# Optimization experiments

Hardware: AMD Instinct MI355X
Metric: run time of the kernel (lower is better)

The kernel has to match this reference:

```python
import jax, jax.numpy as jnp
import numpy as np

B, S = 16, 8192
Q_DIM, K_DIM, ATTN_DIM = 512, 512, 512


def setup_inputs() -> dict:
    key = jax.random.key(0)
    k1, k2, k3, k4, k5, k6 = jax.random.split(key, 6)
    query = jax.random.normal(k1, (B, Q_DIM), dtype=jnp.float32)
    keys = jax.random.normal(k2, (B, S, K_DIM), dtype=jnp.float32)
    mask = jax.random.randint(k3, (B, S), 0, 2, dtype=jnp.int32)
    # learned params (torch Linear stores weight as [out, in]; we keep [in, out])
    Wq = jax.random.normal(k4, (Q_DIM, ATTN_DIM), dtype=jnp.float32) / np.sqrt(Q_DIM)
    Wk = jax.random.normal(k5, (K_DIM, ATTN_DIM), dtype=jnp.float32) / np.sqrt(K_DIM)
    v = jax.random.normal(k6, (ATTN_DIM,), dtype=jnp.float32) / np.sqrt(ATTN_DIM)
    return {"query": query, "keys": keys, "mask": mask, "Wq": Wq, "Wk": Wk, "v": v}


def reference(query, keys, mask, Wq, Wk, v):
    # q: [B, 1, A], k: [B, S, A]
    q = (query @ Wq)[:, None, :]
    k = jnp.einsum('bsk,ka->bsa', keys, Wk)
    # scores e: [B, S]  (v-projection reduces attn dim)
    e = jnp.einsum('bsa,a->bs', jnp.tanh(q + k), v)
    neg_min = jnp.finfo(e.dtype).min
    e = jnp.where(mask == 0, neg_min, e)
    a = jax.nn.softmax(e, axis=-1)  # [B, S]
    c = jnp.einsum('bs,bsk->bk', a, keys)  # context [B, K_DIM]
    return (c, a)
```

## Files before the change

### kernel.cpp

```cpp
#include <hip/hip_runtime.h>

#define BB 16
#define SS 8192
#define DD 512

typedef float  f32x4  __attribute__((ext_vector_type(4)));
typedef __bf16 bf16x8 __attribute__((ext_vector_type(8)));
typedef __bf16 bf16x4 __attribute__((ext_vector_type(4)));

__device__ __forceinline__ void cvt_store_bf4(unsigned short* dst, f32x4 v) {
    bf16x4 o;
    o.x = (__bf16)v.x; o.y = (__bf16)v.y; o.z = (__bf16)v.z; o.w = (__bf16)v.w;
    *(bf16x4*)dst = o;
}

__device__ __forceinline__ float tanh_fast(float x) {
    float e2 = __expf(2.0f * x);
    return 1.0f - 2.0f / (e2 + 1.0f);
}

__global__ __launch_bounds__(256) void prep_kernel(
    const float* __restrict__ query, const float* __restrict__ Wq,
    const float* __restrict__ Wk, float* __restrict__ qproj,
    unsigned short* __restrict__ WkT_f)
{
    __shared__ __bf16 lt[64][65];
    const int bid = blockIdx.x, t = threadIdx.x;
    if (bid < 64) {
        const int k0 = (bid >> 3) * 64, n0 = (bid & 7) * 64;
#pragma unroll
        for (int rep = 0; rep < 4; ++rep) {
            const int k = rep * 16 + (t >> 4), n = (t & 15) * 4;
            f32x4 vv = *(const f32x4*)&Wk[(size_t)(k0 + k) * DD + n0 + n];
            lt[k][n] = (__bf16)vv.x; lt[k][n + 1] = (__bf16)vv.y;
            lt[k][n + 2] = (__bf16)vv.z; lt[k][n + 3] = (__bf16)vv.w;
        }
        __syncthreads();
        const int g_loc = t >> 6, lane = t & 63;
        const int ml = lane & 15, quad = lane >> 4;
        const int g = (bid & 7) * 4 + g_loc;
#pragma unroll
        for (int j_loc = 0; j_loc < 2; ++j_loc) {
            const int j = (bid >> 3) * 2 + j_loc;
            bf16x8 o;
#pragma unroll
            for (int d = 0; d < 8; ++d)
                o[d] = lt[j_loc * 32 + quad * 8 + d][g_loc * 16 + ml];
            *(bf16x8*)&WkT_f[((size_t)((g * 16 + j) * 64 + lane)) * 8] = o;
        }
    } else {
        const int idx = (bid - 64) * 256 + t;
        const int b = idx >> 9;
        const int n = idx & 511;
        const float* q  = query + b * DD;
        const float* wp = Wq + n;
        float acc = 0.0f;
#pragma unroll 8
        for (int k = 0; k < DD; ++k)
            acc = fmaf(q[k], wp[(size_t)k * DD], acc);
        qproj[b * DD + n] = acc;
    }
}

__global__ __launch_bounds__(512, 4) void fused_kernel(
    const float* __restrict__ keys, const unsigned short* __restrict__ WkT_f,
    const float* __restrict__ qproj, const float* __restrict__ vvec,
    const int* __restrict__ mask, float* __restrict__ e_ws,
    float* __restrict__ cpart, float2* __restrict__ ml_ws)
{
    __shared__ unsigned short ksA[16 * 2048];
    __shared__ float sm_part[8][64];
    __shared__ float w_sh[64];
    __shared__ f32x4 red[3][128];

    const int tid  = threadIdx.x;
    const int w    = tid >> 6;
    const int lane = tid & 63;
    const int ml   = lane & 15;
    const int quad = lane >> 4;
    const int bid  = blockIdx.x;
    const int b    = bid >> 7;
    const int chunk = bid & 127;
    const int s0   = chunk << 6;

    const int m  = tid >> 3;
    const int q8 = tid & 7;
    const float* krow = keys + ((size_t)(b * SS + s0 + m)) * DD + q8 * 4;
    const int it = m >> 4;
    const int sq = q8 >> 1;
    const int j0 = (q8 & 1) * 4;
    const int base = it * 512 + ((m & 15) + 16 * sq) * 8 + j0;
    {
        f32x4 kst[8];
#pragma unroll
        for (int h = 0; h < 2; ++h) {
#pragma unroll
            for (int j = 0; j < 8; ++j)
                kst[j] = *(const f32x4*)(krow + (h * 8 + j) * 32);
#pragma unroll
            for (int j = 0; j < 8; ++j)
                cvt_store_bf4(&ksA[(h * 8 + j) * 2048 + base], kst[j]);
        }
    }
    __syncthreads();

    const unsigned short* wfb = WkT_f + (size_t)w * 32768 + lane * 8;

    f32x4 acc[4][4];
#pragma unroll
    for (int i = 0; i < 4; ++i)
#pragma unroll
        for (int jn = 0; jn < 4; ++jn) acc[i][jn] = (f32x4){0.f, 0.f, 0.f, 0.f};

#pragma unroll 4
    for (int j = 0; j < 16; ++j) {
        bf16x8 af[4];
#pragma unroll
        for (int i = 0; i < 4; ++i)
            af[i] = *(const bf16x8*)&ksA[j * 2048 + (i * 64 + lane) * 8];
#pragma unroll
        for (int jn = 0; jn < 4; ++jn) {
            bf16x8 bfr = *(const bf16x8*)(wfb + ((jn * 16 + j) << 9));
#pragma unroll
            for (int i = 0; i < 4; ++i)
                acc[i][jn] = __builtin_amdgcn_mfma_f32_16x16x32_bf16(af[i], bfr, acc[i][jn], 0, 0, 0);
        }
    }

    float qv[4], vv[4];
#pragma unroll
    for (int jn = 0; jn < 4; ++jn) {
        const int n = w * 64 + jn * 16 + ml;
        qv[jn] = qproj[b * DD + n];
        vv[jn] = vvec[n];
    }
#pragma unroll
    for (int i = 0; i < 4; ++i) {
#pragma unroll
        for (int r = 0; r < 4; ++r) {
            float s = 0.0f;
#pragma unroll
            for (int jn = 0; jn < 4; ++jn) {
                float xx = acc[i][jn][r] + qv[jn];
                s += tanh_fast(xx) * vv[jn];
            }
            s += __shfl_xor(s, 1, 64);
            s += __shfl_xor(s, 2, 64);
            s += __shfl_xor(s, 4, 64);
            s += __shfl_xor(s, 8, 64);
            if (ml == 0) sm_part[w][i * 16 + quad * 4 + r] = s;
        }
    }
    __syncthreads();

    if (tid < 64) {
        float e = sm_part[0][tid] + sm_part[1][tid] + sm_part[2][tid] + sm_part[3][tid]
                + sm_part[4][tid] + sm_part[5][tid] + sm_part[6][tid] + sm_part[7][tid];
        const int mk = mask[b * SS + s0 + tid];
        if (mk == 0) e = -3.402823466e38f;
        e_ws[(size_t)b * SS + s0 + tid] = e;
        float mx = e;
#pragma unroll
        for (int off = 32; off >= 1; off >>= 1) mx = fmaxf(mx, __shfl_xor(mx, off, 64));
        float wv = (mk == 0) ? 0.0f : __expf(e - mx);
        float l  = wv;
#pragma unroll
        for (int off = 32; off >= 1; off >>= 1) l += __shfl_xor(l, off, 64);
        w_sh[tid] = wv;
        if (tid == 0) ml_ws[b * 128 + chunk] = make_float2(mx, l);
    }
    __syncthreads();

    const int n4 = (tid & 127) << 2;
    const int sh = tid >> 7;
    const float* kctx = keys + ((size_t)(b * SS + s0 + sh * 16)) * DD + n4;
    f32x4 cacc = (f32x4){0.f, 0.f, 0.f, 0.f};
#pragma unroll 8
    for (int sI = 0; sI < 16; ++sI) {
        float wgt = w_sh[sh * 16 + sI];
        f32x4 kv  = *(const f32x4*)(kctx + (size_t)sI * DD);
        cacc += kv * wgt;
    }
    if (sh) red[sh - 1][tid & 127] = cacc;
    __syncthreads();
    if (sh == 0) {
        cacc += red[0][tid] + red[1][tid] + red[2][tid];
        *(f32x4*)(cpart + ((size_t)(b * 128 + chunk)) * 512 + n4) = cacc;
    }
}

__global__ __launch_bounds__(256) void finalize_kernel(
    const float* __restrict__ e_ws, const float* __restrict__ cpart,
    const float2* __restrict__ ml_ws, float* __restrict__ out)
{
    __shared__ float rm[4], rs[4];
    __shared__ float sc_sh[128];
    __shared__ float cred[4][512];
    const int bid = blockIdx.x, t = threadIdx.x;
    const int b = (bid < 16) ? bid : ((bid - 16) >> 3);

    float mi = -3.402823466e38f, li = 0.0f;
    if (t < 128) { float2 p = ml_ws[b * 128 + t]; mi = p.x; li = p.y; }
    float mr = mi;
#pragma unroll
    for (int off = 32; off >= 1; off >>= 1) mr = fmaxf(mr, __shfl_xor(mr, off, 64));
    if ((t & 63) == 0) rm[t >> 6] = mr;
    __syncthreads();
    const float M = fmaxf(fmaxf(rm[0], rm[1]), fmaxf(rm[2], rm[3]));
    float si = (t < 128) ? li * __expf(mi - M) : 0.0f;
#pragma unroll
    for (int off = 32; off >= 1; off >>= 1) si += __shfl_xor(si, off, 64);
    if ((t & 63) == 0) rs[t >> 6] = si;
    __syncthreads();
    const float L = rs[0] + rs[1] + rs[2] + rs[3];
    const float invL = 1.0f / L;

    if (bid < 16) {
        if (t < 128) sc_sh[t] = __expf(ml_ws[b * 128 + t].x - M);
        __syncthreads();
        const int w2 = t >> 6, l = t & 63;
        float pa[8] = {0.f, 0.f, 0.f, 0.f, 0.f, 0.f, 0.f, 0.f};
#pragma unroll 4
        for (int i = w2 * 32; i < w2 * 32 + 32; ++i) {
            const float sc = sc_sh[i];
            const float* cp = cpart + ((size_t)(b * 128 + i)) * 512 + l * 8;
#pragma unroll
            for (int c = 0; c < 8; ++c) pa[c] = fmaf(cp[c], sc, pa[c]);
        }
#pragma unroll
        for (int c = 0; c < 8; ++c) cred[w2][l * 8 + c] = pa[c];
        __syncthreads();
#pragma unroll
        for (int rep = 0; rep < 2; ++rep) {
            const int n = t + rep * 256;
            out[b * DD + n] = (cred[0][n] + cred[1][n] + cred[2][n] + cred[3][n]) * invL;
        }
    } else {
        const int chunk8 = (bid - 16) & 7;
        const float* ep = e_ws + (size_t)b * SS + chunk8 * 1024;
        float* ap = out + BB * DD + (size_t)b * SS + chunk8 * 1024;
#pragma unroll
        for (int r = 0; r < 4; ++r) {
            float e = ep[t + 256 * r];
            ap[t + 256 * r] = __expf(e - M) * invL;
        }
    }
}

extern "C" void kernel_launch(void* const* d_in, const int* in_sizes, int n_in,
                              void* d_out, int out_size, void* d_ws, size_t ws_size,
                              hipStream_t stream)
{
    const float* query = (const float*)d_in[0];
    const float* keys  = (const float*)d_in[1];
    const int*   mask  = (const int*)  d_in[2];
    const float* Wq    = (const float*)d_in[3];
    const float* Wk    = (const float*)d_in[4];
    const float* v     = (const float*)d_in[5];
    float* out = (float*)d_out;

    float*          qproj = (float*)d_ws;
    unsigned short* WkT_f = (unsigned short*)((char*)d_ws + 32768);
    float*          e_ws  = (float*)((char*)d_ws + 32768 + 524288);
    float*          cpart = (float*)((char*)d_ws + 32768 + 2 * 524288);
    float2*         ml_ws = (float2*)((char*)d_ws + 32768 + 2 * 524288 + 4194304);

    prep_kernel    <<<96, 256, 0, stream>>>(query, Wq, Wk, qproj, WkT_f);
    fused_kernel   <<<BB * (SS / 64), 512, 0, stream>>>(keys, WkT_f, qproj, v, mask,
                                                        e_ws, cpart, ml_ws);
    finalize_kernel<<<16 + 128, 256, 0, stream>>>(e_ws, cpart, ml_ws, out);
}
```

Baseline: 486.1 us.

## Make fused kernel persistent over eight chunks with double-buffered key staging

The fused kernel now launches 256 blocks of 1024 threads, and each block loops over eight 64-row chunks instead of handling one. The next chunk's keys are loaded into registers and written to a second LDS buffer while MFMAs run on the current chunk, so the global load latency overlaps compute. With 16 waves, each wave now covers 32 output columns instead of 64. The trade-offs are fewer blocks (256 on a 256-CU part, one block per CU), double the LDS footprint, and three block-wide barriers per chunk.

```diff
diff --git a/kernel.cpp b/kernel.cpp
--- a/kernel.cpp
+++ b/kernel.cpp
@@ -62,16 +62,16 @@
     }
 }
 
-__global__ __launch_bounds__(512, 4) void fused_kernel(
+__global__ __launch_bounds__(1024, 4) void fused_kernel(
     const float* __restrict__ keys, const unsigned short* __restrict__ WkT_f,
     const float* __restrict__ qproj, const float* __restrict__ vvec,
     const int* __restrict__ mask, float* __restrict__ e_ws,
     float* __restrict__ cpart, float2* __restrict__ ml_ws)
 {
-    __shared__ unsigned short ksA[16 * 2048];
-    __shared__ float sm_part[8][64];
+    __shared__ unsigned short ksA[2][16 * 2048];
+    __shared__ float sm_part[16][64];
     __shared__ float w_sh[64];
-    __shared__ f32x4 red[3][128];
+    __shared__ f32x4 red[7][128];
 
     const int tid  = threadIdx.x;
     const int w    = tid >> 6;
@@ -79,113 +79,129 @@
     const int ml   = lane & 15;
     const int quad = lane >> 4;
     const int bid  = blockIdx.x;
-    const int b    = bid >> 7;
-    const int chunk = bid & 127;
-    const int s0   = chunk << 6;
-
-    const int m  = tid >> 3;
-    const int q8 = tid & 7;
-    const float* krow = keys + ((size_t)(b * SS + s0 + m)) * DD + q8 * 4;
-    const int it = m >> 4;
-    const int sq = q8 >> 1;
-    const int j0 = (q8 & 1) * 4;
-    const int base = it * 512 + ((m & 15) + 16 * sq) * 8 + j0;
-    {
-        f32x4 kst[8];
-#pragma unroll
-        for (int h = 0; h < 2; ++h) {
-#pragma unroll
-            for (int j = 0; j < 8; ++j)
-                kst[j] = *(const f32x4*)(krow + (h * 8 + j) * 32);
-#pragma unroll
-            for (int j = 0; j < 8; ++j)
-                cvt_store_bf4(&ksA[(h * 8 + j) * 2048 + base], kst[j]);
-        }
-    }
-    __syncthreads();
-
-    const unsigned short* wfb = WkT_f + (size_t)w * 32768 + lane * 8;
-
-    f32x4 acc[4][4];
-#pragma unroll
-    for (int i = 0; i < 4; ++i)
-#pragma unroll
-        for (int jn = 0; jn < 4; ++jn) acc[i][jn] = (f32x4){0.f, 0.f, 0.f, 0.f};
-
-#pragma unroll 4
-    for (int j = 0; j < 16; ++j) {
-        bf16x8 af[4];
-#pragma unroll
-        for (int i = 0; i < 4; ++i)
-            af[i] = *(const bf16x8*)&ksA[j * 2048 + (i * 64 + lane) * 8];
-#pragma unroll
-        for (int jn = 0; jn < 4; ++jn) {
-            bf16x8 bfr = *(const bf16x8*)(wfb + ((jn * 16 + j) << 9));
-#pragma unroll
-            for (int i = 0; i < 4; ++i)
-                acc[i][jn] = __builtin_amdgcn_mfma_f32_16x16x32_bf16(af[i], bfr, acc[i][jn], 0, 0, 0);
-        }
-    }
-
-    float qv[4], vv[4];
-#pragma unroll
-    for (int jn = 0; jn < 4; ++jn) {
-        const int n = w * 64 + jn * 16 + ml;
+    const int b    = bid >> 4;
+    const int grp  = bid & 15;
+    const int sgrp = grp << 9;
+
+    const int m   = tid >> 4;
+    const int q16 = tid & 15;
+    const int it  = m >> 4;
+    const int base = it * 512 + ((m & 15) + 16 * ((q16 & 7) >> 1)) * 8 + (q16 & 1) * 4;
+    const int jb  = q16 >> 3;
+    const float* kr = keys + ((size_t)(b * SS + sgrp + m)) * DD + q16 * 4;
+
+    const unsigned short* wfb = WkT_f + (size_t)w * 16384 + lane * 8;
+
+    float qv[2], vv[2];
+#pragma unroll
+    for (int jn = 0; jn < 2; ++jn) {
+        const int n = w * 32 + jn * 16 + ml;
         qv[jn] = qproj[b * DD + n];
         vv[jn] = vvec[n];
     }
-#pragma unroll
-    for (int i = 0; i < 4; ++i) {
-#pragma unroll
-        for (int r = 0; r < 4; ++r) {
-            float s = 0.0f;
-#pragma unroll
-            for (int jn = 0; jn < 4; ++jn) {
-                float xx = acc[i][jn][r] + qv[jn];
-                s += tanh_fast(xx) * vv[jn];
+
+    {
+        f32x4 tmp[8];
+#pragma unroll
+        for (int h = 0; h < 8; ++h) tmp[h] = *(const f32x4*)(kr + h * 64);
+#pragma unroll
+        for (int h = 0; h < 8; ++h) cvt_store_bf4(&ksA[0][(jb + 2 * h) * 2048 + base], tmp[h]);
+    }
+    __syncthreads();
+
+    for (int i = 0; i < 8; ++i) {
+        const int cur = i & 1, nxt = cur ^ 1;
+        const int scur = sgrp + i * 64;
+
+        f32x4 tmp[8];
+        if (i < 7) {
+            const float* krn = kr + (size_t)(i + 1) * 64 * DD;
+#pragma unroll
+            for (int h = 0; h < 8; ++h) tmp[h] = *(const f32x4*)(krn + h * 64);
+        }
+
+        f32x4 acc[4][2];
+#pragma unroll
+        for (int ii = 0; ii < 4; ++ii)
+#pragma unroll
+            for (int jn = 0; jn < 2; ++jn) acc[ii][jn] = (f32x4){0.f, 0.f, 0.f, 0.f};
+
+#pragma unroll 4
+        for (int j = 0; j < 16; ++j) {
+            bf16x8 af[4];
+#pragma unroll
+            for (int ii = 0; ii < 4; ++ii)
+                af[ii] = *(const bf16x8*)&ksA[cur][j * 2048 + (ii * 64 + lane) * 8];
+#pragma unroll
+            for (int jn = 0; jn < 2; ++jn) {
+                bf16x8 bfr = *(const bf16x8*)(wfb + ((jn * 16 + j) << 9));
+#pragma unroll
+                for (int ii = 0; ii < 4; ++ii)
+                    acc[ii][jn] = __builtin_amdgcn_mfma_f32_16x16x32_bf16(af[ii], bfr, acc[ii][jn], 0, 0, 0);
             }
-            s += __shfl_xor(s, 1, 64);
-            s += __shfl_xor(s, 2, 64);
-            s += __shfl_xor(s, 4, 64);
-            s += __shfl_xor(s, 8, 64);
-            if (ml == 0) sm_part[w][i * 16 + quad * 4 + r] = s;
-        }
-    }
-    __syncthreads();
-
-    if (tid < 64) {
-        float e = sm_part[0][tid] + sm_part[1][tid] + sm_part[2][tid] + sm_part[3][tid]
-                + sm_part[4][tid] + sm_part[5][tid] + sm_part[6][tid] + sm_part[7][tid];
-        const int mk = mask[b * SS + s0 + tid];
-        if (mk == 0) e = -3.402823466e38f;
-        e_ws[(size_t)b * SS + s0 + tid] = e;
-        float mx = e;
-#pragma unroll
-        for (int off = 32; off >= 1; off >>= 1) mx = fmaxf(mx, __shfl_xor(mx, off, 64));
-        float wv = (mk == 0) ? 0.0f : __expf(e - mx);
-        float l  = wv;
-#pragma unroll
-        for (int off = 32; off >= 1; off >>= 1) l += __shfl_xor(l, off, 64);
-        w_sh[tid] = wv;
-        if (tid == 0) ml_ws[b * 128 + chunk] = make_float2(mx, l);
-    }
-    __syncthreads();
-
-    const int n4 = (tid & 127) << 2;
-    const int sh = tid >> 7;
-    const float* kctx = keys + ((size_t)(b * SS + s0 + sh * 16)) * DD + n4;
-    f32x4 cacc = (f32x4){0.f, 0.f, 0.f, 0.f};
-#pragma unroll 8
-    for (int sI = 0; sI < 16; ++sI) {
-        float wgt = w_sh[sh * 16 + sI];
-        f32x4 kv  = *(const f32x4*)(kctx + (size_t)sI * DD);
-        cacc += kv * wgt;
-    }
-    if (sh) red[sh - 1][tid & 127] = cacc;
-    __syncthreads();
-    if (sh == 0) {
-        cacc += red[0][tid] + red[1][tid] + red[2][tid];
-        *(f32x4*)(cpart + ((size_t)(b * 128 + chunk)) * 512 + n4) = cacc;
+        }
+
+        if (i < 7) {
+#pragma unroll
+            for (int h = 0; h < 8; ++h)
+                cvt_store_bf4(&ksA[nxt][(jb + 2 * h) * 2048 + base], tmp[h]);
+        }
+
+#pragma unroll
+        for (int ii = 0; ii < 4; ++ii) {
+#pragma unroll
+            for (int r = 0; r < 4; ++r) {
+                float s = 0.0f;
+#pragma unroll
+                for (int jn = 0; jn < 2; ++jn) {
+                    float xx = acc[ii][jn][r] + qv[jn];
+                    s += tanh_fast(xx) * vv[jn];
+                }
+                s += __shfl_xor(s, 1, 64);
+                s += __shfl_xor(s, 2, 64);
+                s += __shfl_xor(s, 4, 64);
+                s += __shfl_xor(s, 8, 64);
+                if (ml == 0) sm_part[w][ii * 16 + quad * 4 + r] = s;
+            }
+        }
+        __syncthreads();
+
+        if (tid < 64) {
+            float e = 0.0f;
+#pragma unroll
+            for (int wv = 0; wv < 16; ++wv) e += sm_part[wv][tid];
+            const int mk = mask[b * SS + scur + tid];
+            if (mk == 0) e = -3.402823466e38f;
+            e_ws[(size_t)b * SS + scur + tid] = e;
+            float mx = e;
+#pragma unroll
+            for (int off = 32; off >= 1; off >>= 1) mx = fmaxf(mx, __shfl_xor(mx, off, 64));
+            float wgt = (mk == 0) ? 0.0f : __expf(e - mx);
+            float l = wgt;
+#pragma unroll
+            for (int off = 32; off >= 1; off >>= 1) l += __shfl_xor(l, off, 64);
+            w_sh[tid] = wgt;
+            if (tid == 0) ml_ws[b * 128 + grp * 8 + i] = make_float2(mx, l);
+        }
+        __syncthreads();
+
+        const int n4 = (tid & 127) << 2;
+        const int sh = tid >> 7;
+        const float* kctx = keys + ((size_t)(b * SS + scur + sh * 8)) * DD + n4;
+        f32x4 cacc = (f32x4){0.f, 0.f, 0.f, 0.f};
+#pragma unroll
+        for (int sI = 0; sI < 8; ++sI) {
+            float wgt = w_sh[sh * 8 + sI];
+            f32x4 kv  = *(const f32x4*)(kctx + (size_t)sI * DD);
+            cacc += kv * wgt;
+        }
+        if (sh) red[sh - 1][tid & 127] = cacc;
+        __syncthreads();
+        if (sh == 0) {
+#pragma unroll
+            for (int g2 = 0; g2 < 7; ++g2) cacc += red[g2][tid];
+            *(f32x4*)(cpart + ((size_t)(b * 128 + grp * 8 + i)) * 512 + n4) = cacc;
+        }
     }
 }
 
@@ -266,7 +282,7 @@
     float2*         ml_ws = (float2*)((char*)d_ws + 32768 + 2 * 524288 + 4194304);
 
     prep_kernel    <<<96, 256, 0, stream>>>(query, Wq, Wk, qproj, WkT_f);
-    fused_kernel   <<<BB * (SS / 64), 512, 0, stream>>>(keys, WkT_f, qproj, v, mask,
-                                                        e_ws, cpart, ml_ws);
+    fused_kernel   <<<256, 1024, 0, stream>>>(keys, WkT_f, qproj, v, mask,
+                                              e_ws, cpart, ml_ws);
     finalize_kernel<<<16 + 128, 256, 0, stream>>>(e_ws, cpart, ml_ws, out);
 }
```

Measured after the change: 539.7 us. +11.0%, slower.

## Process 256 rows per block with double-buffered key tiles and online softmax

Applied to the files above, without the earlier changes.

Each fused block now covers 256 sequence rows in eight 32-row steps instead of 64 rows at once. While the MFMA work runs on the current tile, the next key tile is prefetched into a second LDS buffer, and the context is accumulated with a running max and sum (online softmax rescaling). This cuts the grid from 2048 to 512 blocks, shrinks the partial context and stat buffers four-fold, and lets finalize read only 32 partials per batch. The costs are fewer blocks to hide latency, two extra barriers per step, a serial dependency through the running statistics, and column-wise scalar key reads for the context that are not vectorised.

```diff
diff --git a/kernel.cpp b/kernel.cpp
--- a/kernel.cpp
+++ b/kernel.cpp
@@ -7,16 +7,13 @@
 typedef float  f32x4  __attribute__((ext_vector_type(4)));
 typedef __bf16 bf16x8 __attribute__((ext_vector_type(8)));
 typedef __bf16 bf16x4 __attribute__((ext_vector_type(4)));
+
+#define NEG_HUGE -3.402823466e38f
 
 __device__ __forceinline__ void cvt_store_bf4(unsigned short* dst, f32x4 v) {
     bf16x4 o;
     o.x = (__bf16)v.x; o.y = (__bf16)v.y; o.z = (__bf16)v.z; o.w = (__bf16)v.w;
     *(bf16x4*)dst = o;
-}
-
-__device__ __forceinline__ float tanh_fast(float x) {
-    float e2 = __expf(2.0f * x);
-    return 1.0f - 2.0f / (e2 + 1.0f);
 }
 
 __global__ __launch_bounds__(256) void prep_kernel(
@@ -68,10 +65,12 @@
     const int* __restrict__ mask, float* __restrict__ e_ws,
     float* __restrict__ cpart, float2* __restrict__ ml_ws)
 {
-    __shared__ unsigned short ksA[16 * 2048];
-    __shared__ float sm_part[8][64];
-    __shared__ float w_sh[64];
-    __shared__ f32x4 red[3][128];
+    __shared__ unsigned short ksA[2][16 * 1024];
+    __shared__ float sm_part[8][32];
+    __shared__ float w_sh[32];
+    __shared__ float c_run[512];
+    __shared__ int   mask_sh[256];
+    __shared__ float mrun_sh, lrun_sh, alpha_sh;
 
     const int tid  = threadIdx.x;
     const int w    = tid >> 6;
@@ -79,54 +78,21 @@
     const int ml   = lane & 15;
     const int quad = lane >> 4;
     const int bid  = blockIdx.x;
-    const int b    = bid >> 7;
-    const int chunk = bid & 127;
-    const int s0   = chunk << 6;
-
-    const int m  = tid >> 3;
-    const int q8 = tid & 7;
-    const float* krow = keys + ((size_t)(b * SS + s0 + m)) * DD + q8 * 4;
-    const int it = m >> 4;
-    const int sq = q8 >> 1;
-    const int j0 = (q8 & 1) * 4;
-    const int base = it * 512 + ((m & 15) + 16 * sq) * 8 + j0;
-    {
-        f32x4 kst[8];
-#pragma unroll
-        for (int h = 0; h < 2; ++h) {
-#pragma unroll
-            for (int j = 0; j < 8; ++j)
-                kst[j] = *(const f32x4*)(krow + (h * 8 + j) * 32);
-#pragma unroll
-            for (int j = 0; j < 8; ++j)
-                cvt_store_bf4(&ksA[(h * 8 + j) * 2048 + base], kst[j]);
-        }
-    }
-    __syncthreads();
+    const int b    = bid >> 5;
+    const int g    = bid & 31;
+    const int s0   = g << 8;
+
+    const int m   = tid >> 4;
+    const int q16 = tid & 15;
+    const int stb = ((m >> 4) * 512) + (((m & 15) + 16 * ((q16 >> 1) & 3)) * 8) + (q16 & 1) * 4;
+    const int jt  = q16 >> 3;
+    const float* kr = keys + ((size_t)(b * SS + s0 + m)) * DD + q16 * 4;
+
+    c_run[tid] = 0.0f;
+    if (tid < 256) mask_sh[tid] = mask[b * SS + s0 + tid];
+    if (tid == 0) { mrun_sh = NEG_HUGE; lrun_sh = 0.0f; }
 
     const unsigned short* wfb = WkT_f + (size_t)w * 32768 + lane * 8;
-
-    f32x4 acc[4][4];
-#pragma unroll
-    for (int i = 0; i < 4; ++i)
-#pragma unroll
-        for (int jn = 0; jn < 4; ++jn) acc[i][jn] = (f32x4){0.f, 0.f, 0.f, 0.f};
-
-#pragma unroll 4
-    for (int j = 0; j < 16; ++j) {
-        bf16x8 af[4];
-#pragma unroll
-        for (int i = 0; i < 4; ++i)
-            af[i] = *(const bf16x8*)&ksA[j * 2048 + (i * 64 + lane) * 8];
-#pragma unroll
-        for (int jn = 0; jn < 4; ++jn) {
-            bf16x8 bfr = *(const bf16x8*)(wfb + ((jn * 16 + j) << 9));
-#pragma unroll
-            for (int i = 0; i < 4; ++i)
-                acc[i][jn] = __builtin_amdgcn_mfma_f32_16x16x32_bf16(af[i], bfr, acc[i][jn], 0, 0, 0);
-        }
-    }
-
     float qv[4], vv[4];
 #pragma unroll
     for (int jn = 0; jn < 4; ++jn) {
@@ -134,107 +100,149 @@
         qv[jn] = qproj[b * DD + n];
         vv[jn] = vvec[n];
     }
-#pragma unroll
-    for (int i = 0; i < 4; ++i) {
-#pragma unroll
-        for (int r = 0; r < 4; ++r) {
-            float s = 0.0f;
+    {
+        f32x4 pf[8];
+#pragma unroll
+        for (int h = 0; h < 8; ++h) pf[h] = *(const f32x4*)(kr + h * 64);
+#pragma unroll
+        for (int h = 0; h < 8; ++h) cvt_store_bf4(&ksA[0][(2 * h + jt) * 1024 + stb], pf[h]);
+    }
+    __syncthreads();
+
+    for (int i = 0; i < 8; ++i) {
+        const int cur = i & 1, nxt = cur ^ 1;
+
+        f32x4 pf[8];
+        if (i < 7) {
+            const float* kp = kr + (size_t)(i + 1) * 32 * DD;
+#pragma unroll
+            for (int h = 0; h < 8; ++h) pf[h] = *(const f32x4*)(kp + h * 64);
+        }
+        __builtin_amdgcn_sched_barrier(0);
+
+        f32x4 acc[2][4];
+#pragma unroll
+        for (int it = 0; it < 2; ++it)
+#pragma unroll
+            for (int jn = 0; jn < 4; ++jn) acc[it][jn] = (f32x4){0.f, 0.f, 0.f, 0.f};
+
+#pragma unroll 4
+        for (int j = 0; j < 16; ++j) {
+            bf16x8 af0 = *(const bf16x8*)&ksA[cur][j * 1024 + lane * 8];
+            bf16x8 af1 = *(const bf16x8*)&ksA[cur][j * 1024 + 512 + lane * 8];
 #pragma unroll
             for (int jn = 0; jn < 4; ++jn) {
-                float xx = acc[i][jn][r] + qv[jn];
-                s += tanh_fast(xx) * vv[jn];
-            }
-            s += __shfl_xor(s, 1, 64);
-            s += __shfl_xor(s, 2, 64);
-            s += __shfl_xor(s, 4, 64);
-            s += __shfl_xor(s, 8, 64);
-            if (ml == 0) sm_part[w][i * 16 + quad * 4 + r] = s;
-        }
-    }
+                bf16x8 bfr = *(const bf16x8*)(wfb + ((jn * 16 + j) << 9));
+                acc[0][jn] = __builtin_amdgcn_mfma_f32_16x16x32_bf16(af0, bfr, acc[0][jn], 0, 0, 0);
+                acc[1][jn] = __builtin_amdgcn_mfma_f32_16x16x32_bf16(af1, bfr, acc[1][jn], 0, 0, 0);
+            }
+        }
+
+        if (i < 7) {
+#pragma unroll
+            for (int h = 0; h < 8; ++h)
+                cvt_store_bf4(&ksA[nxt][(2 * h + jt) * 1024 + stb], pf[h]);
+        }
+
+#pragma unroll
+        for (int it = 0; it < 2; ++it) {
+#pragma unroll
+            for (int r = 0; r < 4; ++r) {
+                float s = 0.0f;
+#pragma unroll
+                for (int jn = 0; jn < 4; ++jn) {
+                    float x  = acc[it][jn][r] + qv[jn];
+                    float e2 = __expf(2.0f * x);
+                    float rc = __builtin_amdgcn_rcpf(e2 + 1.0f);
+                    s += vv[jn] - 2.0f * vv[jn] * rc;
+                }
+                s += __shfl_xor(s, 1, 64);
+                s += __shfl_xor(s, 2, 64);
+                s += __shfl_xor(s, 4, 64);
+                s += __shfl_xor(s, 8, 64);
+                if (ml == 0) sm_part[w][it * 16 + quad * 4 + r] = s;
+            }
+        }
+        __syncthreads();
+
+        if (tid < 32) {
+            float e = 0.0f;
+#pragma unroll
+            for (int w8 = 0; w8 < 8; ++w8) e += sm_part[w8][tid];
+            const int mk = mask_sh[i * 32 + tid];
+            if (mk == 0) e = NEG_HUGE;
+            e_ws[(size_t)b * SS + s0 + i * 32 + tid] = e;
+            float mx = e;
+#pragma unroll
+            for (int off = 16; off >= 1; off >>= 1) mx = fmaxf(mx, __shfl_xor(mx, off, 64));
+            float wv = (mk == 0) ? 0.0f : __expf(e - mx);
+            float lc = wv;
+#pragma unroll
+            for (int off = 16; off >= 1; off >>= 1) lc += __shfl_xor(lc, off, 64);
+            const float m_old = mrun_sh;
+            const float m_new = fmaxf(m_old, mx);
+            const float alpha = __expf(m_old - m_new);
+            const float beta  = __expf(mx - m_new);
+            w_sh[tid] = wv * beta;
+            if (tid == 0) {
+                mrun_sh  = m_new;
+                lrun_sh  = lrun_sh * alpha + lc * beta;
+                alpha_sh = alpha;
+            }
+        }
+        __syncthreads();
+
+        {
+            const float alpha = alpha_sh;
+            float cacc = c_run[tid] * alpha;
+            const float* kcol = keys + ((size_t)(b * SS + s0 + i * 32)) * DD + tid;
+#pragma unroll
+            for (int sI = 0; sI < 32; sI += 8) {
+                float kvv[8];
+#pragma unroll
+                for (int u = 0; u < 8; ++u) kvv[u] = kcol[(size_t)(sI + u) * DD];
+#pragma unroll
+                for (int u = 0; u < 8; ++u) cacc = fmaf(w_sh[sI + u], kvv[u], cacc);
+            }
+            c_run[tid] = cacc;
+        }
+    }
+
     __syncthreads();
-
-    if (tid < 64) {
-        float e = sm_part[0][tid] + sm_part[1][tid] + sm_part[2][tid] + sm_part[3][tid]
-                + sm_part[4][tid] + sm_part[5][tid] + sm_part[6][tid] + sm_part[7][tid];
-        const int mk = mask[b * SS + s0 + tid];
-        if (mk == 0) e = -3.402823466e38f;
-        e_ws[(size_t)b * SS + s0 + tid] = e;
-        float mx = e;
-#pragma unroll
-        for (int off = 32; off >= 1; off >>= 1) mx = fmaxf(mx, __shfl_xor(mx, off, 64));
-        float wv = (mk == 0) ? 0.0f : __expf(e - mx);
-        float l  = wv;
-#pragma unroll
-        for (int off = 32; off >= 1; off >>= 1) l += __shfl_xor(l, off, 64);
-        w_sh[tid] = wv;
-        if (tid == 0) ml_ws[b * 128 + chunk] = make_float2(mx, l);
-    }
-    __syncthreads();
-
-    const int n4 = (tid & 127) << 2;
-    const int sh = tid >> 7;
-    const float* kctx = keys + ((size_t)(b * SS + s0 + sh * 16)) * DD + n4;
-    f32x4 cacc = (f32x4){0.f, 0.f, 0.f, 0.f};
-#pragma unroll 8
-    for (int sI = 0; sI < 16; ++sI) {
-        float wgt = w_sh[sh * 16 + sI];
-        f32x4 kv  = *(const f32x4*)(kctx + (size_t)sI * DD);
-        cacc += kv * wgt;
-    }
-    if (sh) red[sh - 1][tid & 127] = cacc;
-    __syncthreads();
-    if (sh == 0) {
-        cacc += red[0][tid] + red[1][tid] + red[2][tid];
-        *(f32x4*)(cpart + ((size_t)(b * 128 + chunk)) * 512 + n4) = cacc;
-    }
+    cpart[(size_t)bid * 512 + tid] = c_run[tid];
+    if (tid == 0) ml_ws[bid] = make_float2(mrun_sh, lrun_sh);
 }
 
 __global__ __launch_bounds__(256) void finalize_kernel(
     const float* __restrict__ e_ws, const float* __restrict__ cpart,
     const float2* __restrict__ ml_ws, float* __restrict__ out)
 {
-    __shared__ float rm[4], rs[4];
-    __shared__ float sc_sh[128];
-    __shared__ float cred[4][512];
     const int bid = blockIdx.x, t = threadIdx.x;
     const int b = (bid < 16) ? bid : ((bid - 16) >> 3);
 
-    float mi = -3.402823466e38f, li = 0.0f;
-    if (t < 128) { float2 p = ml_ws[b * 128 + t]; mi = p.x; li = p.y; }
-    float mr = mi;
-#pragma unroll
-    for (int off = 32; off >= 1; off >>= 1) mr = fmaxf(mr, __shfl_xor(mr, off, 64));
-    if ((t & 63) == 0) rm[t >> 6] = mr;
-    __syncthreads();
-    const float M = fmaxf(fmaxf(rm[0], rm[1]), fmaxf(rm[2], rm[3]));
-    float si = (t < 128) ? li * __expf(mi - M) : 0.0f;
-#pragma unroll
-    for (int off = 32; off >= 1; off >>= 1) si += __shfl_xor(si, off, 64);
-    if ((t & 63) == 0) rs[t >> 6] = si;
-    __syncthreads();
-    const float L = rs[0] + rs[1] + rs[2] + rs[3];
+    float M = NEG_HUGE;
+#pragma unroll
+    for (int g2 = 0; g2 < 32; ++g2) M = fmaxf(M, ml_ws[b * 32 + g2].x);
+    float L = 0.0f;
+#pragma unroll
+    for (int g2 = 0; g2 < 32; ++g2) {
+        float2 p = ml_ws[b * 32 + g2];
+        L += p.y * __expf(p.x - M);
+    }
     const float invL = 1.0f / L;
 
     if (bid < 16) {
-        if (t < 128) sc_sh[t] = __expf(ml_ws[b * 128 + t].x - M);
-        __syncthreads();
-        const int w2 = t >> 6, l = t & 63;
-        float pa[8] = {0.f, 0.f, 0.f, 0.f, 0.f, 0.f, 0.f, 0.f};
+        const int n0 = t * 2;
+        float a0 = 0.0f, a1 = 0.0f;
 #pragma unroll 4
-        for (int i = w2 * 32; i < w2 * 32 + 32; ++i) {
-            const float sc = sc_sh[i];
-            const float* cp = cpart + ((size_t)(b * 128 + i)) * 512 + l * 8;
-#pragma unroll
-            for (int c = 0; c < 8; ++c) pa[c] = fmaf(cp[c], sc, pa[c]);
-        }
-#pragma unroll
-        for (int c = 0; c < 8; ++c) cred[w2][l * 8 + c] = pa[c];
-        __syncthreads();
-#pragma unroll
-        for (int rep = 0; rep < 2; ++rep) {
-            const int n = t + rep * 256;
-            out[b * DD + n] = (cred[0][n] + cred[1][n] + cred[2][n] + cred[3][n]) * invL;
-        }
+        for (int g2 = 0; g2 < 32; ++g2) {
+            const float sc = __expf(ml_ws[b * 32 + g2].x - M);
+            const float* cp = cpart + ((size_t)(b * 32 + g2)) * 512 + n0;
+            a0 = fmaf(cp[0], sc, a0);
+            a1 = fmaf(cp[1], sc, a1);
+        }
+        out[b * DD + n0]     = a0 * invL;
+        out[b * DD + n0 + 1] = a1 * invL;
     } else {
         const int chunk8 = (bid - 16) & 7;
         const float* ep = e_ws + (size_t)b * SS + chunk8 * 1024;
@@ -263,10 +271,10 @@
     unsigned short* WkT_f = (unsigned short*)((char*)d_ws + 32768);
     float*          e_ws  = (float*)((char*)d_ws + 32768 + 524288);
     float*          cpart = (float*)((char*)d_ws + 32768 + 2 * 524288);
-    float2*         ml_ws = (float2*)((char*)d_ws + 32768 + 2 * 524288 + 4194304);
+    float2*         ml_ws = (float2*)((char*)d_ws + 32768 + 2 * 524288 + 1048576);
 
     prep_kernel    <<<96, 256, 0, stream>>>(query, Wq, Wk, qproj, WkT_f);
-    fused_kernel   <<<BB * (SS / 64), 512, 0, stream>>>(keys, WkT_f, qproj, v, mask,
-                                                        e_ws, cpart, ml_ws);
+    fused_kernel   <<<512, 512, 0, stream>>>(keys, WkT_f, qproj, v, mask,
+                                             e_ws, cpart, ml_ws);
     finalize_kernel<<<16 + 128, 256, 0, stream>>>(e_ws, cpart, ml_ws, out);
 }
```

Result: slower. 538.0 us (+10.7%).
